# Kernel optimization log

Measured on AMD Instinct MI355X. Metric: run time of the kernel, lower is better.

Reference implementation:

```python
import jax, jax.numpy as jnp
import numpy as np

B, T, D = 4, 50, 512
SRC, SENTS, WORDS = 400, 16, 40
NEG = jnp.float32(-1e30)  # stands in for -inf mask fill (numerically identical post-softmax)


def _seq_mask(lengths, max_len):
    # [n, max_len] bool, True where position < length
    return jnp.arange(max_len)[None, :] < lengths[:, None]


def _mlp_score(q, h, Wq, bq, Uc, v):
    # Bahdanau additive score: v^T tanh(W q + U h)
    # q: [b,t,d], h: [b,s,d] -> [b,t,s]
    wq = q @ Wq + bq                       # [b,t,d]
    uh = h @ Uc                            # [b,s,d]
    wquh = jnp.tanh(wq[:, :, None, :] + uh[:, None, :, :])  # [b,t,s,d]
    return jnp.einsum('btsd,d->bts', wquh, v)


def setup_inputs() -> dict:
    key = jax.random.key(0)
    ks = jax.random.split(key, 20)
    s = np.float32(1.0 / np.sqrt(D))
    def p(k, shape):
        return jax.random.normal(k, shape, jnp.float32) * s
    return {
        'source': jax.random.normal(ks[0], (B, T, D), jnp.float32),
        'src_bank': jax.random.normal(ks[1], (SRC, B, D), jnp.float32),
        'src_lengths': jax.random.randint(ks[2], (B,), 1, SRC + 1),
        'qa_sent_bank': jax.random.normal(ks[3], (SENTS, B, D), jnp.float32),
        'qa_sent_lengths': jax.random.randint(ks[4], (B,), 1, SENTS + 1),
        'qa_word_bank': jax.random.normal(ks[5], (WORDS, B, SENTS, D), jnp.float32),
        'qa_word_lengths': jax.random.randint(ks[6], (B, SENTS), 1, WORDS + 1),
        'Wq_word': p(ks[7], (D, D)), 'bq_word': jnp.zeros((D,), jnp.float32),
        'Uc_word': p(ks[8], (D, D)), 'v_word': p(ks[9], (D,)),
        'Wq_sent': p(ks[10], (D, D)), 'bq_sent': jnp.zeros((D,), jnp.float32),
        'Uc_sent': p(ks[11], (D, D)), 'v_sent': p(ks[12], (D,)),
        'Wq_pass': p(ks[13], (D, D)), 'bq_pass': jnp.zeros((D,), jnp.float32),
        'Uc_pass': p(ks[14], (D, D)), 'v_pass': p(ks[15], (D,)),
    }


def _forward(source, src_bank, qa_sent_bank, qa_word_bank,
             Wq_word, bq_word, Uc_word, v_word,
             Wq_sent, bq_sent, Uc_sent, v_sent,
             Wq_pass, bq_pass, Uc_pass, v_pass,
             src_lengths, qa_word_lengths):
    b = source.shape[0]
    # [words,b,sents,d] -> [b,sents,words,d] -> [b, sents*words, d]
    qa_word = jnp.transpose(qa_word_bank, (1, 2, 0, 3)).reshape(b, SENTS * WORDS, D)
    src = jnp.transpose(src_bank, (1, 0, 2))       # [b,src,d]
    sent = jnp.transpose(qa_sent_bank, (1, 0, 2))  # [b,sents,d]

    qa_word_align = _mlp_score(source, qa_word, Wq_word, bq_word, Uc_word, v_word)  # [b,t,sents*words]
    src_align = _mlp_score(source, src, Wq_pass, bq_pass, Uc_pass, v_pass)          # [b,t,src]
    qa_sent_align = _mlp_score(source, sent, Wq_sent, bq_sent, Uc_sent, v_sent)     # [b,t,sents]

    # hierarchical combination: word score scaled by its sentence score
    qa_hier = (qa_word_align.reshape(b, T, SENTS, WORDS)
               * qa_sent_align[..., None]).reshape(b, T, SENTS * WORDS)

    align = jnp.concatenate([src_align, qa_hier], axis=-1)  # [b,t,src+sents*words]

    qa_mask = _seq_mask(qa_word_lengths.reshape(-1), WORDS).reshape(b, SENTS * WORDS)[:, None, :]
    src_mask = _seq_mask(src_lengths, SRC)[:, None, :]
    mask = jnp.concatenate([src_mask, qa_mask], axis=-1)

    align = jnp.where(mask, align, NEG)
    align_vectors = jax.nn.softmax(align, axis=-1)  # joint length-masked softmax

    memory = jnp.concatenate([src, qa_word], axis=1)          # [b, src+sents*words, d]
    c = jnp.einsum('bts,bsd->btd', align_vectors, memory)     # weighted context sum
    return c


def reference(source, src_bank, src_lengths, qa_sent_bank, qa_sent_lengths,
              qa_word_bank, qa_word_lengths,
              Wq_word, bq_word, Uc_word, v_word,
              Wq_sent, bq_sent, Uc_sent, v_sent,
              Wq_pass, bq_pass, Uc_pass, v_pass):
    # qa_sent_lengths is accepted but unused, matching the original forward()
    return _forward(source, src_bank, qa_sent_bank, qa_word_bank,
                    Wq_word, bq_word, Uc_word, v_word,
                    Wq_sent, bq_sent, Uc_sent, v_sent,
                    Wq_pass, bq_pass, Uc_pass, v_pass,
                    src_lengths, qa_word_lengths)
```

## Files before the change

### kernel.cpp

```cpp
#include <hip/hip_runtime.h>
#include <hip/hip_bf16.h>


#define B_    4
#define T_    50
#define D_    512
#define SRC_  400
#define SENTS_ 16
#define WORDS_ 40
#define NW_   640
#define NMEM_ 1040
#define NK_   1056
#define NJOB_ 1056

#define C2L2E 2.8853900817779268f

typedef unsigned short ushort_t;
using s8v = __attribute__((ext_vector_type(8))) short;
using f4v = __attribute__((ext_vector_type(4))) float;

#define OFF_WQ_WORD 0
#define OFF_WQ_SENT 102400
#define OFF_WQ_PASS 204800
#define OFF_UH_SRC  307200
#define OFF_UH_WORD 1126400
#define OFF_UH_SENT 2437120
#define OFF_SC_SRC  2469888
#define OFF_SC_WORD 2549888
#define OFF_SC_SENT 2677888
#define P_BYTE_OFF  10724352ull
#define MT_BYTE_OFF 11265024ull
#define WT_BYTE_OFF 15590400ull

__device__ __forceinline__ ushort_t f2b(float f) {
    __hip_bfloat16 h = __float2bfloat16(f);
    return *(ushort_t*)&h;
}

__global__ __launch_bounds__(256) void k0f_transpose(
    const float* __restrict__ w0, const float* __restrict__ w1,
    const float* __restrict__ w2, const float* __restrict__ w3,
    const float* __restrict__ w4, const float* __restrict__ w5,
    const float* __restrict__ src_bank, const float* __restrict__ qa_word_bank,
    ushort_t* __restrict__ wt, ushort_t* __restrict__ mt)
{
    __shared__ float tile[32][33];
    int z = blockIdx.z;
    int tx = threadIdx.x & 31, ty = threadIdx.x >> 5;
    if (z < 6) {
        if (blockIdx.x >= 16) return;
        const float* W;
        switch (z) {
            case 0: W = w0; break; case 1: W = w1; break; case 2: W = w2; break;
            case 3: W = w3; break; case 4: W = w4; break; default: W = w5; break;
        }
        ushort_t* Wt = wt + z * (D_ * D_);
        int n0 = blockIdx.x * 32, k0 = blockIdx.y * 32;
#pragma unroll
        for (int a = 0; a < 4; ++a)
            tile[ty + a * 8][tx] = W[(k0 + ty + a * 8) * D_ + n0 + tx];
        __syncthreads();
#pragma unroll
        for (int a = 0; a < 4; ++a)
            Wt[(n0 + ty + a * 8) * D_ + k0 + tx] = f2b(tile[tx][ty + a * 8]);
    } else {
        int b = z - 6;
        int s0 = blockIdx.x * 32, d0 = blockIdx.y * 32;
#pragma unroll
        for (int a = 0; a < 4; ++a) {
            int s = s0 + ty + a * 8;
            float val = 0.f;
            if (s < SRC_) {
                val = src_bank[(s * B_ + b) * D_ + d0 + tx];
            } else if (s < NMEM_) {
                int j = s - SRC_; int se = j / WORDS_; int wd = j - se * WORDS_;
                val = qa_word_bank[((wd * B_ + b) * SENTS_ + se) * D_ + d0 + tx];
            }
            tile[ty + a * 8][tx] = val;
        }
        __syncthreads();
        ushort_t* base = mt + (size_t)b * D_ * NK_;
#pragma unroll
        for (int a = 0; a < 4; ++a) {
            int d = d0 + ty + a * 8;
            base[(size_t)d * NK_ + s0 + tx] = f2b(tile[tx][ty + a * 8]);
        }
    }
}

__global__ __launch_bounds__(256) void k1_gemm(
    const float* __restrict__ source, const float* __restrict__ src_bank,
    const float* __restrict__ qa_sent_bank, const float* __restrict__ qa_word_bank,
    const ushort_t* __restrict__ wt,
    const float* __restrict__ bq_word, const float* __restrict__ bq_sent,
    const float* __restrict__ bq_pass,
    float* __restrict__ wsf)
{
    __shared__ short At[64 * 32];
    __shared__ short Bt[64 * 32];
    int z = blockIdx.z;
    int M, atype; const float* bias; float* C;
    switch (z) {
        case 0: M = 200;  atype = 0; bias = bq_word; C = wsf + OFF_WQ_WORD; break;
        case 1: M = 200;  atype = 0; bias = bq_sent; C = wsf + OFF_WQ_SENT; break;
        case 2: M = 200;  atype = 0; bias = bq_pass; C = wsf + OFF_WQ_PASS; break;
        case 3: M = 2560; atype = 1; bias = nullptr; C = wsf + OFF_UH_WORD; break;
        case 4: M = 1600; atype = 2; bias = nullptr; C = wsf + OFF_UH_SRC;  break;
        default: M = 64;  atype = 3; bias = nullptr; C = wsf + OFF_UH_SENT; break;
    }
    int m0 = blockIdx.y * 64;
    if (m0 >= M) return;
    int n0 = blockIdx.x * 64;
    const ushort_t* W = wt + z * (D_ * D_);

    int tid = threadIdx.x;
    int lane = tid & 63, wv = tid >> 6;
    int quad = lane >> 4, l16 = lane & 15;
    int sm = tid >> 2, koff = (tid & 3) * 8;

    const float* arow = nullptr;
    {
        int r = m0 + sm;
        if (r < M) {
            if (atype == 0) arow = source + r * D_;
            else if (atype == 1) { int b = r / NW_; int j = r - b * NW_;
                                   int se = j / WORDS_; int wd = j - se * WORDS_;
                                   arow = qa_word_bank + ((wd * B_ + b) * SENTS_ + se) * D_; }
            else if (atype == 2) { int b = r / SRC_; int j = r - b * SRC_;
                                   arow = src_bank + (j * B_ + b) * D_; }
            else                 { int b = r >> 4; int s2 = r & 15;
                                   arow = qa_sent_bank + (s2 * B_ + b) * D_; }
        }
    }
    const ushort_t* wrow = W + (n0 + sm) * D_;

    f4v acc[4] = { {0.f,0.f,0.f,0.f}, {0.f,0.f,0.f,0.f},
                   {0.f,0.f,0.f,0.f}, {0.f,0.f,0.f,0.f} };

    for (int kk = 0; kk < 16; ++kk) {
        int k0 = kk * 32;
        union { ushort_t u[8]; int4 v; } pk;
        if (arow) {
            float4 f0 = *(const float4*)(arow + k0 + koff);
            float4 f1 = *(const float4*)(arow + k0 + koff + 4);
            pk.u[0] = f2b(f0.x); pk.u[1] = f2b(f0.y);
            pk.u[2] = f2b(f0.z); pk.u[3] = f2b(f0.w);
            pk.u[4] = f2b(f1.x); pk.u[5] = f2b(f1.y);
            pk.u[6] = f2b(f1.z); pk.u[7] = f2b(f1.w);
        } else {
            pk.v = int4{0, 0, 0, 0};
        }
        int4 bv = *(const int4*)(wrow + k0 + koff);
        *(int4*)(At + sm * 32 + koff) = pk.v;
        *(int4*)(Bt + sm * 32 + koff) = bv;
        __syncthreads();
        s8v af = *(const s8v*)(At + (wv * 16 + l16) * 32 + quad * 8);
#pragma unroll
        for (int ng = 0; ng < 4; ++ng) {
            s8v bf = *(const s8v*)(Bt + (ng * 16 + l16) * 32 + quad * 8);
            acc[ng] = __builtin_amdgcn_mfma_f32_16x16x32_bf16(af, bf, acc[ng], 0, 0, 0);
        }
        __syncthreads();
    }
#pragma unroll
    for (int ng = 0; ng < 4; ++ng) {
        int col = n0 + ng * 16 + l16;
        float bb = bias ? bias[col] : 0.f;
#pragma unroll
        for (int rr = 0; rr < 4; ++rr) {
            int row = m0 + wv * 16 + quad * 4 + rr;
            if (row < M) C[row * D_ + col] = (acc[ng][rr] + bb) * C2L2E;
        }
    }
}

__global__ __launch_bounds__(256) void k2_scores(
    const float* __restrict__ v_word, const float* __restrict__ v_sent,
    const float* __restrict__ v_pass,
    const int* __restrict__ src_lengths, const int* __restrict__ qa_word_lengths,
    float* __restrict__ wsf)
{
    int lane = threadIdx.x & 63;
    int job2 = blockIdx.x * 4 + (threadIdx.x >> 6);
    int job = job2 >> 1, th = job2 & 1;
    int b = job / NJOB_, slot = job - b * NJOB_;
    const float* uh; const float* v; const float* wq; float* out; int ostride;
    if (slot < SRC_) {
        if (slot >= src_lengths[b]) return;
        uh = wsf + OFF_UH_SRC + (b * SRC_ + slot) * D_;
        v = v_pass; wq = wsf + OFF_WQ_PASS + b * T_ * D_;
        out = wsf + OFF_SC_SRC + b * T_ * SRC_ + slot; ostride = SRC_;
    } else if (slot < NMEM_) {
        int j = slot - SRC_;
        int se = j / WORDS_; int wd = j - se * WORDS_;
        if (wd >= qa_word_lengths[b * SENTS_ + se]) return;
        uh = wsf + OFF_UH_WORD + (b * NW_ + j) * D_;
        v = v_word; wq = wsf + OFF_WQ_WORD + b * T_ * D_;
        out = wsf + OFF_SC_WORD + b * T_ * NW_ + j; ostride = NW_;
    } else {
        int s2 = slot - NMEM_;
        uh = wsf + OFF_UH_SENT + (b * SENTS_ + s2) * D_;
        v = v_sent; wq = wsf + OFF_WQ_SENT + b * T_ * D_;
        out = wsf + OFF_SC_SENT + b * T_ * SENTS_ + s2; ostride = SENTS_;
    }
    int d0 = lane * 8;
    float4 u0 = *(const float4*)(uh + d0);
    float4 u1 = *(const float4*)(uh + d0 + 4);
    float uhr[8] = {u0.x, u0.y, u0.z, u0.w, u1.x, u1.y, u1.z, u1.w};
    float4 v0 = *(const float4*)(v + d0);
    float4 v1 = *(const float4*)(v + d0 + 4);
    float vr[8] = {v0.x, v0.y, v0.z, v0.w, v1.x, v1.y, v1.z, v1.w};

    float vs = ((vr[0] + vr[1]) + (vr[2] + vr[3])) + ((vr[4] + vr[5]) + (vr[6] + vr[7]));
#pragma unroll
    for (int off = 32; off > 0; off >>= 1) vs += __shfl_xor(vs, off, 64);

    const float* wqh = wq + th * 25 * D_;
    float acc[25];
#pragma unroll 1
    for (int c = 0; c < 5; ++c) {
#pragma unroll
        for (int u5 = 0; u5 < 5; ++u5) {
            int u = c * 5 + u5;
            const float* wr = wqh + u * D_ + d0;
            float4 w0 = *(const float4*)(wr);
            float4 w1 = *(const float4*)(wr + 4);
            float wrr[8] = {w0.x, w0.y, w0.z, w0.w, w1.x, w1.y, w1.z, w1.w};
            float a = 0.f;
#pragma unroll
            for (int j = 0; j < 8; ++j) {
                float e = __builtin_amdgcn_exp2f(wrr[j] + uhr[j]);
                float r = __builtin_amdgcn_rcpf(e + 1.f);
                a = fmaf(vr[j], r, a);
            }
            acc[u] = a;
        }
    }
#pragma unroll
    for (int off = 32; off > 0; off >>= 1) {
#pragma unroll
        for (int u = 0; u < 25; ++u)
            acc[u] += __shfl_xor(acc[u], off, 64);
    }
    if (lane == 0) {
#pragma unroll
        for (int u = 0; u < 25; ++u)
            out[(th * 25 + u) * ostride] = fmaf(-2.f, acc[u], vs);
    }
}

__global__ __launch_bounds__(256) void k3a_softmax(
    const int* __restrict__ src_lengths, const int* __restrict__ qa_word_lengths,
    const float* __restrict__ wsf, ushort_t* __restrict__ P)
{
    __shared__ float p[NMEM_];
    __shared__ float red[4];
    int tid = threadIdx.x, lane = tid & 63, wv = tid >> 6;
    int bt = blockIdx.x, b = bt / T_, t = bt - b * T_;
    const float* sc_src  = wsf + OFF_SC_SRC  + bt * SRC_;
    const float* sc_word = wsf + OFF_SC_WORD + bt * NW_;
    const float* sc_sent = wsf + OFF_SC_SENT + bt * SENTS_;
    int slen = src_lengths[b];
    float mx = -3.0e38f;
    for (int j = tid; j < NMEM_; j += 256) {
        float val;
        if (j < SRC_) {
            val = (j < slen) ? sc_src[j] : -1e30f;
        } else {
            int jj = j - SRC_; int se = jj / WORDS_; int wd = jj - se * WORDS_;
            float raw = sc_word[jj] * sc_sent[se];
            val = (wd < qa_word_lengths[b * SENTS_ + se]) ? raw : -1e30f;
        }
        p[j] = val;
        mx = fmaxf(mx, val);
    }
#pragma unroll
    for (int off = 32; off > 0; off >>= 1) mx = fmaxf(mx, __shfl_xor(mx, off, 64));
    if (lane == 0) red[wv] = mx;
    __syncthreads();
    mx = fmaxf(fmaxf(red[0], red[1]), fmaxf(red[2], red[3]));
    __syncthreads();
    float lsum = 0.f;
    for (int j = tid; j < NMEM_; j += 256) {
        float e = __expf(p[j] - mx);
        p[j] = e; lsum += e;
    }
#pragma unroll
    for (int off = 32; off > 0; off >>= 1) lsum += __shfl_xor(lsum, off, 64);
    if (lane == 0) red[wv] = lsum;
    __syncthreads();
    float inv = 1.f / (red[0] + red[1] + red[2] + red[3]);
    ushort_t* prow = P + (size_t)(b * 64 + t) * NK_;
    for (int j = tid; j < NK_; j += 256)
        prow[j] = (j < NMEM_) ? f2b(p[j] * inv) : (ushort_t)0;
}

__global__ __launch_bounds__(256) void k3c_gemm(
    const ushort_t* __restrict__ P, const ushort_t* __restrict__ Mt,
    float* __restrict__ out)
{
    __shared__ short At[64 * 32];
    __shared__ short Bt[32 * 32];
    int b = blockIdx.y;
    int n0 = blockIdx.x * 32;
    int tid = threadIdx.x;
    int lane = tid & 63, wv = tid >> 6;
    int quad = lane >> 4, l16 = lane & 15;
    int smA = tid >> 2, koffA = (tid & 3) * 8;
    int smB = tid >> 3, koffB = (tid & 7) * 4;

    const ushort_t* arow = P + (size_t)(b * 64 + smA) * NK_ + koffA;
    const ushort_t* brow = Mt + ((size_t)(b * D_ + n0 + smB)) * NK_ + koffB;

    f4v acc[2] = { {0.f,0.f,0.f,0.f}, {0.f,0.f,0.f,0.f} };

    for (int kk = 0; kk < 33; ++kk) {
        int k0 = kk * 32;
        int4 av = *(const int4*)(arow + k0);
        int2 bv = *(const int2*)(brow + k0);
        *(int4*)(At + smA * 32 + koffA) = av;
        *(int2*)(Bt + smB * 32 + koffB) = bv;
        __syncthreads();
        s8v af = *(const s8v*)(At + (wv * 16 + l16) * 32 + quad * 8);
#pragma unroll
        for (int ng = 0; ng < 2; ++ng) {
            s8v bf = *(const s8v*)(Bt + (ng * 16 + l16) * 32 + quad * 8);
            acc[ng] = __builtin_amdgcn_mfma_f32_16x16x32_bf16(af, bf, acc[ng], 0, 0, 0);
        }
        __syncthreads();
    }
#pragma unroll
    for (int ng = 0; ng < 2; ++ng) {
        int col = n0 + ng * 16 + l16;
#pragma unroll
        for (int rr = 0; rr < 4; ++rr) {
            int row = wv * 16 + quad * 4 + rr;
            if (row < T_) out[(size_t)(b * T_ + row) * D_ + col] = acc[ng][rr];
        }
    }
}

extern "C" void kernel_launch(void* const* d_in, const int* in_sizes, int n_in,
                              void* d_out, int out_size, void* d_ws, size_t ws_size,
                              hipStream_t stream)
{
    (void)in_sizes; (void)n_in; (void)out_size; (void)ws_size;
    const float* source          = (const float*)d_in[0];
    const float* src_bank        = (const float*)d_in[1];
    const int*   src_lengths     = (const int*)d_in[2];
    const float* qa_sent_bank    = (const float*)d_in[3];
    const float* qa_word_bank    = (const float*)d_in[5];
    const int*   qa_word_lengths = (const int*)d_in[6];
    const float* Wq_word = (const float*)d_in[7];
    const float* bq_word = (const float*)d_in[8];
    const float* Uc_word = (const float*)d_in[9];
    const float* v_word  = (const float*)d_in[10];
    const float* Wq_sent = (const float*)d_in[11];
    const float* bq_sent = (const float*)d_in[12];
    const float* Uc_sent = (const float*)d_in[13];
    const float* v_sent  = (const float*)d_in[14];
    const float* Wq_pass = (const float*)d_in[15];
    const float* bq_pass = (const float*)d_in[16];
    const float* Uc_pass = (const float*)d_in[17];
    const float* v_pass  = (const float*)d_in[18];

    float* wsf = (float*)d_ws;
    ushort_t* Pb  = (ushort_t*)((char*)d_ws + P_BYTE_OFF);
    ushort_t* mt  = (ushort_t*)((char*)d_ws + MT_BYTE_OFF);
    ushort_t* wt  = (ushort_t*)((char*)d_ws + WT_BYTE_OFF);
    float* out = (float*)d_out;

    k0f_transpose<<<dim3(33, 16, 10), dim3(256), 0, stream>>>(
        Wq_word, Wq_sent, Wq_pass, Uc_word, Uc_pass, Uc_sent,
        src_bank, qa_word_bank, wt, mt);
    k1_gemm<<<dim3(8, 40, 6), dim3(256), 0, stream>>>(
        source, src_bank, qa_sent_bank, qa_word_bank, wt,
        bq_word, bq_sent, bq_pass, wsf);
    k2_scores<<<dim3(NJOB_ * 2), dim3(256), 0, stream>>>(
        v_word, v_sent, v_pass, src_lengths, qa_word_lengths, wsf);
    k3a_softmax<<<dim3(200), dim3(256), 0, stream>>>(src_lengths, qa_word_lengths, wsf, Pb);
    k3c_gemm<<<dim3(16, 4), dim3(256), 0, stream>>>(Pb, mt, out);
}
```

Measured before the change: 166.3 us.

## Merge five kernel launches into one cooperative persistent kernel with grid syncs

Replaces the five separate kernels (transpose, projection GEMM, score, softmax, context GEMM) with one cooperative persistent kernel. Blocks loop over job indices in each phase, and the phases are separated by grid.sync(). The grid is sized from the occupancy query and capped at 1024 blocks. This removes the launch overhead and the gaps between kernels, at the cost of grid-wide barrier latency and less parallelism in phases with few jobs. The occupancy query also runs on the host on every call.

```diff
diff --git a/kernel.cpp b/kernel.cpp
--- a/kernel.cpp
+++ b/kernel.cpp
@@ -1,6 +1,9 @@
 #include <hip/hip_runtime.h>
 #include <hip/hip_bf16.h>
-
+#include <hip/hip_cooperative_groups.h>
+
+
+namespace cg = cooperative_groups;
 
 #define B_    4
 #define T_    50
@@ -37,305 +40,303 @@
     return *(ushort_t*)&h;
 }
 
-__global__ __launch_bounds__(256) void k0f_transpose(
+__global__ __launch_bounds__(256, 2) void mega(
+    const float* __restrict__ source, const float* __restrict__ src_bank,
+    const int* __restrict__ src_lengths,
+    const float* __restrict__ qa_sent_bank, const float* __restrict__ qa_word_bank,
+    const int* __restrict__ qa_word_lengths,
     const float* __restrict__ w0, const float* __restrict__ w1,
     const float* __restrict__ w2, const float* __restrict__ w3,
     const float* __restrict__ w4, const float* __restrict__ w5,
-    const float* __restrict__ src_bank, const float* __restrict__ qa_word_bank,
-    ushort_t* __restrict__ wt, ushort_t* __restrict__ mt)
-{
-    __shared__ float tile[32][33];
-    int z = blockIdx.z;
-    int tx = threadIdx.x & 31, ty = threadIdx.x >> 5;
-    if (z < 6) {
-        if (blockIdx.x >= 16) return;
-        const float* W;
-        switch (z) {
-            case 0: W = w0; break; case 1: W = w1; break; case 2: W = w2; break;
-            case 3: W = w3; break; case 4: W = w4; break; default: W = w5; break;
-        }
-        ushort_t* Wt = wt + z * (D_ * D_);
-        int n0 = blockIdx.x * 32, k0 = blockIdx.y * 32;
-#pragma unroll
-        for (int a = 0; a < 4; ++a)
-            tile[ty + a * 8][tx] = W[(k0 + ty + a * 8) * D_ + n0 + tx];
-        __syncthreads();
-#pragma unroll
-        for (int a = 0; a < 4; ++a)
-            Wt[(n0 + ty + a * 8) * D_ + k0 + tx] = f2b(tile[tx][ty + a * 8]);
-    } else {
-        int b = z - 6;
-        int s0 = blockIdx.x * 32, d0 = blockIdx.y * 32;
-#pragma unroll
-        for (int a = 0; a < 4; ++a) {
-            int s = s0 + ty + a * 8;
-            float val = 0.f;
-            if (s < SRC_) {
-                val = src_bank[(s * B_ + b) * D_ + d0 + tx];
-            } else if (s < NMEM_) {
-                int j = s - SRC_; int se = j / WORDS_; int wd = j - se * WORDS_;
-                val = qa_word_bank[((wd * B_ + b) * SENTS_ + se) * D_ + d0 + tx];
-            }
-            tile[ty + a * 8][tx] = val;
-        }
-        __syncthreads();
-        ushort_t* base = mt + (size_t)b * D_ * NK_;
-#pragma unroll
-        for (int a = 0; a < 4; ++a) {
-            int d = d0 + ty + a * 8;
-            base[(size_t)d * NK_ + s0 + tx] = f2b(tile[tx][ty + a * 8]);
-        }
-    }
-}
-
-__global__ __launch_bounds__(256) void k1_gemm(
-    const float* __restrict__ source, const float* __restrict__ src_bank,
-    const float* __restrict__ qa_sent_bank, const float* __restrict__ qa_word_bank,
-    const ushort_t* __restrict__ wt,
     const float* __restrict__ bq_word, const float* __restrict__ bq_sent,
     const float* __restrict__ bq_pass,
-    float* __restrict__ wsf)
-{
-    __shared__ short At[64 * 32];
-    __shared__ short Bt[64 * 32];
-    int z = blockIdx.z;
-    int M, atype; const float* bias; float* C;
-    switch (z) {
-        case 0: M = 200;  atype = 0; bias = bq_word; C = wsf + OFF_WQ_WORD; break;
-        case 1: M = 200;  atype = 0; bias = bq_sent; C = wsf + OFF_WQ_SENT; break;
-        case 2: M = 200;  atype = 0; bias = bq_pass; C = wsf + OFF_WQ_PASS; break;
-        case 3: M = 2560; atype = 1; bias = nullptr; C = wsf + OFF_UH_WORD; break;
-        case 4: M = 1600; atype = 2; bias = nullptr; C = wsf + OFF_UH_SRC;  break;
-        default: M = 64;  atype = 3; bias = nullptr; C = wsf + OFF_UH_SENT; break;
-    }
-    int m0 = blockIdx.y * 64;
-    if (m0 >= M) return;
-    int n0 = blockIdx.x * 64;
-    const ushort_t* W = wt + z * (D_ * D_);
-
-    int tid = threadIdx.x;
-    int lane = tid & 63, wv = tid >> 6;
-    int quad = lane >> 4, l16 = lane & 15;
-    int sm = tid >> 2, koff = (tid & 3) * 8;
-
-    const float* arow = nullptr;
-    {
-        int r = m0 + sm;
-        if (r < M) {
-            if (atype == 0) arow = source + r * D_;
-            else if (atype == 1) { int b = r / NW_; int j = r - b * NW_;
-                                   int se = j / WORDS_; int wd = j - se * WORDS_;
-                                   arow = qa_word_bank + ((wd * B_ + b) * SENTS_ + se) * D_; }
-            else if (atype == 2) { int b = r / SRC_; int j = r - b * SRC_;
-                                   arow = src_bank + (j * B_ + b) * D_; }
-            else                 { int b = r >> 4; int s2 = r & 15;
-                                   arow = qa_sent_bank + (s2 * B_ + b) * D_; }
-        }
-    }
-    const ushort_t* wrow = W + (n0 + sm) * D_;
-
-    f4v acc[4] = { {0.f,0.f,0.f,0.f}, {0.f,0.f,0.f,0.f},
-                   {0.f,0.f,0.f,0.f}, {0.f,0.f,0.f,0.f} };
-
-    for (int kk = 0; kk < 16; ++kk) {
-        int k0 = kk * 32;
-        union { ushort_t u[8]; int4 v; } pk;
-        if (arow) {
-            float4 f0 = *(const float4*)(arow + k0 + koff);
-            float4 f1 = *(const float4*)(arow + k0 + koff + 4);
-            pk.u[0] = f2b(f0.x); pk.u[1] = f2b(f0.y);
-            pk.u[2] = f2b(f0.z); pk.u[3] = f2b(f0.w);
-            pk.u[4] = f2b(f1.x); pk.u[5] = f2b(f1.y);
-            pk.u[6] = f2b(f1.z); pk.u[7] = f2b(f1.w);
-        } else {
-            pk.v = int4{0, 0, 0, 0};
-        }
-        int4 bv = *(const int4*)(wrow + k0 + koff);
-        *(int4*)(At + sm * 32 + koff) = pk.v;
-        *(int4*)(Bt + sm * 32 + koff) = bv;
-        __syncthreads();
-        s8v af = *(const s8v*)(At + (wv * 16 + l16) * 32 + quad * 8);
-#pragma unroll
-        for (int ng = 0; ng < 4; ++ng) {
-            s8v bf = *(const s8v*)(Bt + (ng * 16 + l16) * 32 + quad * 8);
-            acc[ng] = __builtin_amdgcn_mfma_f32_16x16x32_bf16(af, bf, acc[ng], 0, 0, 0);
-        }
-        __syncthreads();
-    }
-#pragma unroll
-    for (int ng = 0; ng < 4; ++ng) {
-        int col = n0 + ng * 16 + l16;
-        float bb = bias ? bias[col] : 0.f;
-#pragma unroll
-        for (int rr = 0; rr < 4; ++rr) {
-            int row = m0 + wv * 16 + quad * 4 + rr;
-            if (row < M) C[row * D_ + col] = (acc[ng][rr] + bb) * C2L2E;
-        }
-    }
-}
-
-__global__ __launch_bounds__(256) void k2_scores(
     const float* __restrict__ v_word, const float* __restrict__ v_sent,
     const float* __restrict__ v_pass,
-    const int* __restrict__ src_lengths, const int* __restrict__ qa_word_lengths,
-    float* __restrict__ wsf)
-{
-    int lane = threadIdx.x & 63;
-    int job2 = blockIdx.x * 4 + (threadIdx.x >> 6);
-    int job = job2 >> 1, th = job2 & 1;
-    int b = job / NJOB_, slot = job - b * NJOB_;
-    const float* uh; const float* v; const float* wq; float* out; int ostride;
-    if (slot < SRC_) {
-        if (slot >= src_lengths[b]) return;
-        uh = wsf + OFF_UH_SRC + (b * SRC_ + slot) * D_;
-        v = v_pass; wq = wsf + OFF_WQ_PASS + b * T_ * D_;
-        out = wsf + OFF_SC_SRC + b * T_ * SRC_ + slot; ostride = SRC_;
-    } else if (slot < NMEM_) {
-        int j = slot - SRC_;
-        int se = j / WORDS_; int wd = j - se * WORDS_;
-        if (wd >= qa_word_lengths[b * SENTS_ + se]) return;
-        uh = wsf + OFF_UH_WORD + (b * NW_ + j) * D_;
-        v = v_word; wq = wsf + OFF_WQ_WORD + b * T_ * D_;
-        out = wsf + OFF_SC_WORD + b * T_ * NW_ + j; ostride = NW_;
-    } else {
-        int s2 = slot - NMEM_;
-        uh = wsf + OFF_UH_SENT + (b * SENTS_ + s2) * D_;
-        v = v_sent; wq = wsf + OFF_WQ_SENT + b * T_ * D_;
-        out = wsf + OFF_SC_SENT + b * T_ * SENTS_ + s2; ostride = SENTS_;
-    }
-    int d0 = lane * 8;
-    float4 u0 = *(const float4*)(uh + d0);
-    float4 u1 = *(const float4*)(uh + d0 + 4);
-    float uhr[8] = {u0.x, u0.y, u0.z, u0.w, u1.x, u1.y, u1.z, u1.w};
-    float4 v0 = *(const float4*)(v + d0);
-    float4 v1 = *(const float4*)(v + d0 + 4);
-    float vr[8] = {v0.x, v0.y, v0.z, v0.w, v1.x, v1.y, v1.z, v1.w};
-
-    float vs = ((vr[0] + vr[1]) + (vr[2] + vr[3])) + ((vr[4] + vr[5]) + (vr[6] + vr[7]));
-#pragma unroll
-    for (int off = 32; off > 0; off >>= 1) vs += __shfl_xor(vs, off, 64);
-
-    const float* wqh = wq + th * 25 * D_;
-    float acc[25];
-#pragma unroll 1
-    for (int c = 0; c < 5; ++c) {
-#pragma unroll
-        for (int u5 = 0; u5 < 5; ++u5) {
-            int u = c * 5 + u5;
-            const float* wr = wqh + u * D_ + d0;
-            float4 w0 = *(const float4*)(wr);
-            float4 w1 = *(const float4*)(wr + 4);
-            float wrr[8] = {w0.x, w0.y, w0.z, w0.w, w1.x, w1.y, w1.z, w1.w};
-            float a = 0.f;
-#pragma unroll
-            for (int j = 0; j < 8; ++j) {
-                float e = __builtin_amdgcn_exp2f(wrr[j] + uhr[j]);
-                float r = __builtin_amdgcn_rcpf(e + 1.f);
-                a = fmaf(vr[j], r, a);
-            }
-            acc[u] = a;
-        }
-    }
-#pragma unroll
-    for (int off = 32; off > 0; off >>= 1) {
-#pragma unroll
-        for (int u = 0; u < 25; ++u)
-            acc[u] += __shfl_xor(acc[u], off, 64);
-    }
-    if (lane == 0) {
-#pragma unroll
-        for (int u = 0; u < 25; ++u)
-            out[(th * 25 + u) * ostride] = fmaf(-2.f, acc[u], vs);
-    }
-}
-
-__global__ __launch_bounds__(256) void k3a_softmax(
-    const int* __restrict__ src_lengths, const int* __restrict__ qa_word_lengths,
-    const float* __restrict__ wsf, ushort_t* __restrict__ P)
-{
-    __shared__ float p[NMEM_];
-    __shared__ float red[4];
-    int tid = threadIdx.x, lane = tid & 63, wv = tid >> 6;
-    int bt = blockIdx.x, b = bt / T_, t = bt - b * T_;
-    const float* sc_src  = wsf + OFF_SC_SRC  + bt * SRC_;
-    const float* sc_word = wsf + OFF_SC_WORD + bt * NW_;
-    const float* sc_sent = wsf + OFF_SC_SENT + bt * SENTS_;
-    int slen = src_lengths[b];
-    float mx = -3.0e38f;
-    for (int j = tid; j < NMEM_; j += 256) {
-        float val;
-        if (j < SRC_) {
-            val = (j < slen) ? sc_src[j] : -1e30f;
-        } else {
-            int jj = j - SRC_; int se = jj / WORDS_; int wd = jj - se * WORDS_;
-            float raw = sc_word[jj] * sc_sent[se];
-            val = (wd < qa_word_lengths[b * SENTS_ + se]) ? raw : -1e30f;
-        }
-        p[j] = val;
-        mx = fmaxf(mx, val);
-    }
-#pragma unroll
-    for (int off = 32; off > 0; off >>= 1) mx = fmaxf(mx, __shfl_xor(mx, off, 64));
-    if (lane == 0) red[wv] = mx;
-    __syncthreads();
-    mx = fmaxf(fmaxf(red[0], red[1]), fmaxf(red[2], red[3]));
-    __syncthreads();
-    float lsum = 0.f;
-    for (int j = tid; j < NMEM_; j += 256) {
-        float e = __expf(p[j] - mx);
-        p[j] = e; lsum += e;
-    }
-#pragma unroll
-    for (int off = 32; off > 0; off >>= 1) lsum += __shfl_xor(lsum, off, 64);
-    if (lane == 0) red[wv] = lsum;
-    __syncthreads();
-    float inv = 1.f / (red[0] + red[1] + red[2] + red[3]);
-    ushort_t* prow = P + (size_t)(b * 64 + t) * NK_;
-    for (int j = tid; j < NK_; j += 256)
-        prow[j] = (j < NMEM_) ? f2b(p[j] * inv) : (ushort_t)0;
-}
-
-__global__ __launch_bounds__(256) void k3c_gemm(
-    const ushort_t* __restrict__ P, const ushort_t* __restrict__ Mt,
+    float* __restrict__ wsf, ushort_t* __restrict__ Pg,
+    ushort_t* __restrict__ Mtg, ushort_t* __restrict__ Wtg,
     float* __restrict__ out)
 {
-    __shared__ short At[64 * 32];
-    __shared__ short Bt[32 * 32];
-    int b = blockIdx.y;
-    int n0 = blockIdx.x * 32;
-    int tid = threadIdx.x;
-    int lane = tid & 63, wv = tid >> 6;
-    int quad = lane >> 4, l16 = lane & 15;
-    int smA = tid >> 2, koffA = (tid & 3) * 8;
-    int smB = tid >> 3, koffB = (tid & 7) * 4;
-
-    const ushort_t* arow = P + (size_t)(b * 64 + smA) * NK_ + koffA;
-    const ushort_t* brow = Mt + ((size_t)(b * D_ + n0 + smB)) * NK_ + koffB;
-
-    f4v acc[2] = { {0.f,0.f,0.f,0.f}, {0.f,0.f,0.f,0.f} };
-
-    for (int kk = 0; kk < 33; ++kk) {
-        int k0 = kk * 32;
-        int4 av = *(const int4*)(arow + k0);
-        int2 bv = *(const int2*)(brow + k0);
-        *(int4*)(At + smA * 32 + koffA) = av;
-        *(int2*)(Bt + smB * 32 + koffB) = bv;
-        __syncthreads();
-        s8v af = *(const s8v*)(At + (wv * 16 + l16) * 32 + quad * 8);
-#pragma unroll
-        for (int ng = 0; ng < 2; ++ng) {
-            s8v bf = *(const s8v*)(Bt + (ng * 16 + l16) * 32 + quad * 8);
-            acc[ng] = __builtin_amdgcn_mfma_f32_16x16x32_bf16(af, bf, acc[ng], 0, 0, 0);
-        }
-        __syncthreads();
-    }
-#pragma unroll
-    for (int ng = 0; ng < 2; ++ng) {
-        int col = n0 + ng * 16 + l16;
-#pragma unroll
-        for (int rr = 0; rr < 4; ++rr) {
-            int row = wv * 16 + quad * 4 + rr;
-            if (row < T_) out[(size_t)(b * T_ + row) * D_ + col] = acc[ng][rr];
+    cg::grid_group grid = cg::this_grid();
+    __shared__ __align__(16) char smem[8448];
+    const int tid = threadIdx.x;
+    const int lane = tid & 63, wv = tid >> 6;
+    const int quad = lane >> 4, l16 = lane & 15;
+
+    {
+        float (*tile)[33] = (float(*)[33])smem;
+        int tx = tid & 31, ty = tid >> 5;
+        for (int job = blockIdx.x; job < 3648; job += gridDim.x) {
+            if (job < 1536) {
+                int z = job >> 8, t = job & 255;
+                int n0 = (t & 15) * 32, k0 = (t >> 4) * 32;
+                const float* W;
+                switch (z) { case 0: W = w0; break; case 1: W = w1; break;
+                             case 2: W = w2; break; case 3: W = w3; break;
+                             case 4: W = w4; break; default: W = w5; break; }
+                ushort_t* Wt = Wtg + z * (D_ * D_);
+#pragma unroll
+                for (int a = 0; a < 4; ++a)
+                    tile[ty + a * 8][tx] = W[(k0 + ty + a * 8) * D_ + n0 + tx];
+                __syncthreads();
+#pragma unroll
+                for (int a = 0; a < 4; ++a)
+                    Wt[(n0 + ty + a * 8) * D_ + k0 + tx] = f2b(tile[tx][ty + a * 8]);
+            } else {
+                int j = job - 1536;
+                int b = j / 528, r = j - b * 528;
+                int s0 = (r % 33) * 32, d0 = (r / 33) * 32;
+#pragma unroll
+                for (int a = 0; a < 4; ++a) {
+                    int s = s0 + ty + a * 8;
+                    float val = 0.f;
+                    if (s < SRC_) {
+                        val = src_bank[(s * B_ + b) * D_ + d0 + tx];
+                    } else if (s < NMEM_) {
+                        int jj = s - SRC_; int se = jj / WORDS_; int wd = jj - se * WORDS_;
+                        val = qa_word_bank[((wd * B_ + b) * SENTS_ + se) * D_ + d0 + tx];
+                    }
+                    tile[ty + a * 8][tx] = val;
+                }
+                __syncthreads();
+                ushort_t* base = Mtg + (size_t)b * D_ * NK_;
+#pragma unroll
+                for (int a = 0; a < 4; ++a)
+                    base[(size_t)(d0 + ty + a * 8) * NK_ + s0 + tx] = f2b(tile[tx][ty + a * 8]);
+            }
+            __syncthreads();
+        }
+    }
+    grid.sync();
+
+    {
+        short* At = (short*)smem;
+        short* Bt = (short*)(smem + 4096);
+        int sm = tid >> 2, koff = (tid & 3) * 8;
+        for (int job = blockIdx.x; job < 624; job += gridDim.x) {
+            int z, mt, nt;
+            if (job < 96)       { z = job / 32; int r = job & 31; mt = r >> 3; nt = r & 7; }
+            else if (job < 416) { z = 3; int r = job - 96;  mt = r >> 3; nt = r & 7; }
+            else if (job < 616) { z = 4; int r = job - 416; mt = r >> 3; nt = r & 7; }
+            else                { z = 5; mt = 0; nt = job - 616; }
+            int M, atype; const float* bias; float* C;
+            switch (z) {
+                case 0: M = 200;  atype = 0; bias = bq_word; C = wsf + OFF_WQ_WORD; break;
+                case 1: M = 200;  atype = 0; bias = bq_sent; C = wsf + OFF_WQ_SENT; break;
+                case 2: M = 200;  atype = 0; bias = bq_pass; C = wsf + OFF_WQ_PASS; break;
+                case 3: M = 2560; atype = 1; bias = nullptr; C = wsf + OFF_UH_WORD; break;
+                case 4: M = 1600; atype = 2; bias = nullptr; C = wsf + OFF_UH_SRC;  break;
+                default: M = 64;  atype = 3; bias = nullptr; C = wsf + OFF_UH_SENT; break;
+            }
+            int m0 = mt * 64, n0 = nt * 64;
+            const ushort_t* W = Wtg + z * (D_ * D_);
+            const float* arow = nullptr;
+            {
+                int r = m0 + sm;
+                if (r < M) {
+                    if (atype == 0) arow = source + r * D_;
+                    else if (atype == 1) { int b = r / NW_; int jj = r - b * NW_;
+                                           int se = jj / WORDS_; int wd = jj - se * WORDS_;
+                                           arow = qa_word_bank + ((wd * B_ + b) * SENTS_ + se) * D_; }
+                    else if (atype == 2) { int b = r / SRC_; int jj = r - b * SRC_;
+                                           arow = src_bank + (jj * B_ + b) * D_; }
+                    else                 { int b = r >> 4; int s2 = r & 15;
+                                           arow = qa_sent_bank + (s2 * B_ + b) * D_; }
+                }
+            }
+            const ushort_t* wrow = W + (n0 + sm) * D_;
+            f4v acc[4] = { {0.f,0.f,0.f,0.f}, {0.f,0.f,0.f,0.f},
+                           {0.f,0.f,0.f,0.f}, {0.f,0.f,0.f,0.f} };
+            for (int kk = 0; kk < 16; ++kk) {
+                int k0 = kk * 32;
+                union { ushort_t u[8]; int4 v; } pk;
+                if (arow) {
+                    float4 f0 = *(const float4*)(arow + k0 + koff);
+                    float4 f1 = *(const float4*)(arow + k0 + koff + 4);
+                    pk.u[0] = f2b(f0.x); pk.u[1] = f2b(f0.y);
+                    pk.u[2] = f2b(f0.z); pk.u[3] = f2b(f0.w);
+                    pk.u[4] = f2b(f1.x); pk.u[5] = f2b(f1.y);
+                    pk.u[6] = f2b(f1.z); pk.u[7] = f2b(f1.w);
+                } else {
+                    pk.v = int4{0, 0, 0, 0};
+                }
+                int4 bv = *(const int4*)(wrow + k0 + koff);
+                *(int4*)(At + sm * 32 + koff) = pk.v;
+                *(int4*)(Bt + sm * 32 + koff) = bv;
+                __syncthreads();
+                s8v af = *(const s8v*)(At + (wv * 16 + l16) * 32 + quad * 8);
+#pragma unroll
+                for (int ng = 0; ng < 4; ++ng) {
+                    s8v bf = *(const s8v*)(Bt + (ng * 16 + l16) * 32 + quad * 8);
+                    acc[ng] = __builtin_amdgcn_mfma_f32_16x16x32_bf16(af, bf, acc[ng], 0, 0, 0);
+                }
+                __syncthreads();
+            }
+#pragma unroll
+            for (int ng = 0; ng < 4; ++ng) {
+                int col = n0 + ng * 16 + l16;
+                float bb = bias ? bias[col] : 0.f;
+#pragma unroll
+                for (int rr = 0; rr < 4; ++rr) {
+                    int row = m0 + wv * 16 + quad * 4 + rr;
+                    if (row < M) C[row * D_ + col] = (acc[ng][rr] + bb) * C2L2E;
+                }
+            }
+        }
+    }
+    grid.sync();
+
+    {
+        for (int job2 = blockIdx.x * 4 + wv; job2 < 8448; job2 += gridDim.x * 4) {
+            int job = job2 >> 1, th = job2 & 1;
+            int b = job / NJOB_, slot = job - b * NJOB_;
+            const float* uh; const float* v; const float* wq; float* sco; int ostride;
+            bool active = true;
+            if (slot < SRC_) {
+                active = (slot < src_lengths[b]);
+                uh = wsf + OFF_UH_SRC + (b * SRC_ + slot) * D_;
+                v = v_pass; wq = wsf + OFF_WQ_PASS + b * T_ * D_;
+                sco = wsf + OFF_SC_SRC + b * T_ * SRC_ + slot; ostride = SRC_;
+            } else if (slot < NMEM_) {
+                int j = slot - SRC_;
+                int se = j / WORDS_; int wd = j - se * WORDS_;
+                active = (wd < qa_word_lengths[b * SENTS_ + se]);
+                uh = wsf + OFF_UH_WORD + (b * NW_ + j) * D_;
+                v = v_word; wq = wsf + OFF_WQ_WORD + b * T_ * D_;
+                sco = wsf + OFF_SC_WORD + b * T_ * NW_ + j; ostride = NW_;
+            } else {
+                int s2 = slot - NMEM_;
+                uh = wsf + OFF_UH_SENT + (b * SENTS_ + s2) * D_;
+                v = v_sent; wq = wsf + OFF_WQ_SENT + b * T_ * D_;
+                sco = wsf + OFF_SC_SENT + b * T_ * SENTS_ + s2; ostride = SENTS_;
+            }
+            if (!active) continue;
+            int d0 = lane * 8;
+            float4 u0 = *(const float4*)(uh + d0);
+            float4 u1 = *(const float4*)(uh + d0 + 4);
+            float uhr[8] = {u0.x, u0.y, u0.z, u0.w, u1.x, u1.y, u1.z, u1.w};
+            float4 v0 = *(const float4*)(v + d0);
+            float4 v1 = *(const float4*)(v + d0 + 4);
+            float vr[8] = {v0.x, v0.y, v0.z, v0.w, v1.x, v1.y, v1.z, v1.w};
+            float vs = ((vr[0] + vr[1]) + (vr[2] + vr[3])) + ((vr[4] + vr[5]) + (vr[6] + vr[7]));
+#pragma unroll
+            for (int off = 32; off > 0; off >>= 1) vs += __shfl_xor(vs, off, 64);
+            const float* wqh = wq + th * 25 * D_;
+            float acc[25];
+#pragma unroll 1
+            for (int c = 0; c < 5; ++c) {
+#pragma unroll
+                for (int u5 = 0; u5 < 5; ++u5) {
+                    int u = c * 5 + u5;
+                    const float* wr = wqh + u * D_ + d0;
+                    float4 wq0 = *(const float4*)(wr);
+                    float4 wq1 = *(const float4*)(wr + 4);
+                    float wrr[8] = {wq0.x, wq0.y, wq0.z, wq0.w, wq1.x, wq1.y, wq1.z, wq1.w};
+                    float a = 0.f;
+#pragma unroll
+                    for (int j = 0; j < 8; ++j) {
+                        float e = __builtin_amdgcn_exp2f(wrr[j] + uhr[j]);
+                        float r = __builtin_amdgcn_rcpf(e + 1.f);
+                        a = fmaf(vr[j], r, a);
+                    }
+                    acc[u] = a;
+                }
+            }
+#pragma unroll
+            for (int off = 32; off > 0; off >>= 1) {
+#pragma unroll
+                for (int u = 0; u < 25; ++u)
+                    acc[u] += __shfl_xor(acc[u], off, 64);
+            }
+            if (lane == 0) {
+#pragma unroll
+                for (int u = 0; u < 25; ++u)
+                    sco[(th * 25 + u) * ostride] = fmaf(-2.f, acc[u], vs);
+            }
+        }
+    }
+    grid.sync();
+
+    {
+        float* p = (float*)smem;
+        float* red = (float*)(smem + 4160);
+        for (int bt = blockIdx.x; bt < 200; bt += gridDim.x) {
+            int b = bt / T_, t = bt - b * T_;
+            const float* sc_src  = wsf + OFF_SC_SRC  + bt * SRC_;
+            const float* sc_word = wsf + OFF_SC_WORD + bt * NW_;
+            const float* sc_sent = wsf + OFF_SC_SENT + bt * SENTS_;
+            int slen = src_lengths[b];
+            float mx = -3.0e38f;
+            for (int j = tid; j < NMEM_; j += 256) {
+                float val;
+                if (j < SRC_) {
+                    val = (j < slen) ? sc_src[j] : -1e30f;
+                } else {
+                    int jj = j - SRC_; int se = jj / WORDS_; int wd = jj - se * WORDS_;
+                    float raw = sc_word[jj] * sc_sent[se];
+                    val = (wd < qa_word_lengths[b * SENTS_ + se]) ? raw : -1e30f;
+                }
+                p[j] = val;
+                mx = fmaxf(mx, val);
+            }
+#pragma unroll
+            for (int off = 32; off > 0; off >>= 1) mx = fmaxf(mx, __shfl_xor(mx, off, 64));
+            if (lane == 0) red[wv] = mx;
+            __syncthreads();
+            mx = fmaxf(fmaxf(red[0], red[1]), fmaxf(red[2], red[3]));
+            __syncthreads();
+            float lsum = 0.f;
+            for (int j = tid; j < NMEM_; j += 256) {
+                float e = __expf(p[j] - mx);
+                p[j] = e; lsum += e;
+            }
+#pragma unroll
+            for (int off = 32; off > 0; off >>= 1) lsum += __shfl_xor(lsum, off, 64);
+            if (lane == 0) red[wv] = lsum;
+            __syncthreads();
+            float inv = 1.f / (red[0] + red[1] + red[2] + red[3]);
+            ushort_t* prow = Pg + (size_t)(b * 64 + t) * NK_;
+            for (int j = tid; j < NK_; j += 256)
+                prow[j] = (j < NMEM_) ? f2b(p[j] * inv) : (ushort_t)0;
+            __syncthreads();
+        }
+    }
+    grid.sync();
+
+    {
+        short* At = (short*)smem;
+        short* Bt = (short*)(smem + 4096);
+        int smA = tid >> 2, koffA = (tid & 3) * 8;
+        int smB = tid >> 3, koffB = (tid & 7) * 4;
+        for (int job = blockIdx.x; job < 64; job += gridDim.x) {
+            int b = job >> 4, nt = job & 15;
+            int n0 = nt * 32;
+            const ushort_t* arow = Pg + (size_t)(b * 64 + smA) * NK_ + koffA;
+            const ushort_t* brow = Mtg + ((size_t)(b * D_ + n0 + smB)) * NK_ + koffB;
+            f4v acc[2] = { {0.f,0.f,0.f,0.f}, {0.f,0.f,0.f,0.f} };
+            for (int kk = 0; kk < 33; ++kk) {
+                int k0 = kk * 32;
+                int4 av = *(const int4*)(arow + k0);
+                int2 bv = *(const int2*)(brow + k0);
+                *(int4*)(At + smA * 32 + koffA) = av;
+                *(int2*)(Bt + smB * 32 + koffB) = bv;
+                __syncthreads();
+                s8v af = *(const s8v*)(At + (wv * 16 + l16) * 32 + quad * 8);
+#pragma unroll
+                for (int ng = 0; ng < 2; ++ng) {
+                    s8v bf = *(const s8v*)(Bt + (ng * 16 + l16) * 32 + quad * 8);
+                    acc[ng] = __builtin_amdgcn_mfma_f32_16x16x32_bf16(af, bf, acc[ng], 0, 0, 0);
+                }
+                __syncthreads();
+            }
+#pragma unroll
+            for (int ng = 0; ng < 2; ++ng) {
+                int col = n0 + ng * 16 + l16;
+#pragma unroll
+                for (int rr = 0; rr < 4; ++rr) {
+                    int row = wv * 16 + quad * 4 + rr;
+                    if (row < T_) out[(size_t)(b * T_ + row) * D_ + col] = acc[ng][rr];
+                }
+            }
         }
     }
 }
@@ -370,14 +371,25 @@
     ushort_t* wt  = (ushort_t*)((char*)d_ws + WT_BYTE_OFF);
     float* out = (float*)d_out;
 
-    k0f_transpose<<<dim3(33, 16, 10), dim3(256), 0, stream>>>(
-        Wq_word, Wq_sent, Wq_pass, Uc_word, Uc_pass, Uc_sent,
-        src_bank, qa_word_bank, wt, mt);
-    k1_gemm<<<dim3(8, 40, 6), dim3(256), 0, stream>>>(
-        source, src_bank, qa_sent_bank, qa_word_bank, wt,
-        bq_word, bq_sent, bq_pass, wsf);
-    k2_scores<<<dim3(NJOB_ * 2), dim3(256), 0, stream>>>(
-        v_word, v_sent, v_pass, src_lengths, qa_word_lengths, wsf);
-    k3a_softmax<<<dim3(200), dim3(256), 0, stream>>>(src_lengths, qa_word_lengths, wsf, Pb);
-    k3c_gemm<<<dim3(16, 4), dim3(256), 0, stream>>>(Pb, mt, out);
+    int nb = 0;
+    hipError_t oerr = hipOccupancyMaxActiveBlocksPerMultiprocessor(&nb, mega, 256, 0);
+    if (oerr != hipSuccess || nb < 1) nb = 1;
+    int ncu = 0, dev = 0;
+    if (hipGetDevice(&dev) != hipSuccess ||
+        hipDeviceGetAttribute(&ncu, hipDeviceAttributeMultiprocessorCount, dev) != hipSuccess ||
+        ncu < 1) ncu = 256;
+    int gridn = nb * ncu;
+    if (gridn > 1024) gridn = 1024;
+    if (gridn < 1) gridn = 1;
+
+    void* args[] = {
+        (void*)&source, (void*)&src_bank, (void*)&src_lengths,
+        (void*)&qa_sent_bank, (void*)&qa_word_bank, (void*)&qa_word_lengths,
+        (void*)&Wq_word, (void*)&Wq_sent, (void*)&Wq_pass,
+        (void*)&Uc_word, (void*)&Uc_pass, (void*)&Uc_sent,
+        (void*)&bq_word, (void*)&bq_sent, (void*)&bq_pass,
+        (void*)&v_word, (void*)&v_sent, (void*)&v_pass,
+        (void*)&wsf, (void*)&Pb, (void*)&mt, (void*)&wt, (void*)&out
+    };
+    hipLaunchCooperativeKernel((void*)mega, dim3(gridn), dim3(256), args, 0, stream);
 }
```

Result: slower. 455.8 us (+174.1%).
